# Kernel optimization log

Hardware: AMD Instinct MI355X
Metric: run time of the kernel (lower is better)

Reference implementation:

```python
import jax, jax.numpy as jnp
import numpy as np

HID = 128
N_NODES = 50000
N_EDGES = 640000
N_GRAPHS = 64
N_LAYERS = 3
LN_EPS = 1e-5


def _ln(h, g, b):
    mu = jnp.mean(h, axis=-1, keepdims=True)
    v = jnp.mean(jnp.square(h - mu), axis=-1, keepdims=True)
    return (h - mu) * jax.lax.rsqrt(v + LN_EPS) * g + b


def _mlp2(h, W1, b1, g, be, W2, b2):
    # Linear -> ReLU -> LayerNorm -> (Dropout=identity in eval) -> Linear
    h = _ln(jax.nn.relu(h @ W1.T + b1), g, be)
    return h @ W2.T + b2


def _forward(x, edge_index, batch, axis_W1, axis_b1, axis_g, axis_be, axis_W2, axis_b2, org_W1, org_b1, org_g, org_be, org_W2, org_b2, nin_W, nin_b, conv_W1, conv_b1, conv_g, conv_be, conv_W2, conv_b2, eps, ln_g, ln_b, gate_W1, gate_b1, gate_g, gate_be, gate_W2, gate_b2, head_W1, head_b1, head_g, head_be, head_W2, head_b2):
    axis = x[:, 9:12]
    origin = x[:, 12:15]
    others = jnp.concatenate([x[:, :9], x[:, 15:19]], axis=1)  # [N, 13]
    axis_z = _mlp2(axis, axis_W1, axis_b1, axis_g, axis_be, axis_W2, axis_b2)
    org_z = _mlp2(origin, org_W1, org_b1, org_g, org_be, org_W2, org_b2)
    h = jnp.concatenate([others, axis_z, org_z], axis=1) @ nin_W.T + nin_b  # [N, HID]
    src, dst = edge_index[0], edge_index[1]
    n = x.shape[0]
    for l in range(N_LAYERS):
        res = h
        # GIN: sum-aggregate source features into targets (gather + scatter-add)
        agg = jax.ops.segment_sum(h[src], dst, num_segments=n)
        m = (1.0 + eps[l]) * h + agg
        m = _mlp2(m, conv_W1[l], conv_b1[l], conv_g[l], conv_be[l], conv_W2[l], conv_b2[l])
        h = _ln(jax.nn.relu(m), ln_g[l], ln_b[l]) + res
    # AttentionalAggregation: segment softmax over per-graph node gates
    gate = _mlp2(h, gate_W1, gate_b1, gate_g, gate_be, gate_W2, gate_b2)  # [N, 1]
    gmax = jax.ops.segment_max(gate, batch, num_segments=N_GRAPHS)
    e = jnp.exp(gate - gmax[batch])
    denom = jax.ops.segment_sum(e, batch, num_segments=N_GRAPHS)
    attn = e / denom[batch]
    g = jax.ops.segment_sum(attn * h, batch, num_segments=N_GRAPHS)  # [B, HID]
    logit = _mlp2(g, head_W1, head_b1, head_g, head_be, head_W2, head_b2)[:, 0]
    return logit


def setup_inputs() -> dict:
    key = jax.random.key(0)
    ks = iter(jax.random.split(key, 64))
    nk = lambda: next(ks)
    lin = lambda o, i: jax.random.normal(nk(), (o, i), jnp.float32) / np.float32(np.sqrt(i))
    lin3 = lambda L, o, i: jnp.stack([lin(o, i) for _ in range(L)])
    z = lambda *s: jnp.zeros(s, jnp.float32)
    o = lambda *s: jnp.ones(s, jnp.float32)
    inp = {}
    inp['x'] = jax.random.normal(nk(), (N_NODES, 19), jnp.float32)
    inp['edge_index'] = jax.random.randint(nk(), (2, N_EDGES), 0, N_NODES)
    inp['batch'] = jnp.sort(jax.random.randint(nk(), (N_NODES,), 0, N_GRAPHS))
    for p in ('axis', 'org'):
        inp[p + '_W1'] = lin(16, 3); inp[p + '_b1'] = z(16)
        inp[p + '_g'] = o(16); inp[p + '_be'] = z(16)
        inp[p + '_W2'] = lin(16, 16); inp[p + '_b2'] = z(16)
    inp['nin_W'] = lin(HID, 45); inp['nin_b'] = z(HID)
    inp['conv_W1'] = lin3(N_LAYERS, HID, HID); inp['conv_b1'] = z(N_LAYERS, HID)
    inp['conv_g'] = o(N_LAYERS, HID); inp['conv_be'] = z(N_LAYERS, HID)
    inp['conv_W2'] = lin3(N_LAYERS, HID, HID); inp['conv_b2'] = z(N_LAYERS, HID)
    inp['eps'] = z(N_LAYERS)
    inp['ln_g'] = o(N_LAYERS, HID); inp['ln_b'] = z(N_LAYERS, HID)
    for p in ('gate', 'head'):
        inp[p + '_W1'] = lin(HID // 2, HID); inp[p + '_b1'] = z(HID // 2)
        inp[p + '_g'] = o(HID // 2); inp[p + '_be'] = z(HID // 2)
        inp[p + '_W2'] = lin(1, HID // 2); inp[p + '_b2'] = z(1)
    return inp


def reference(x, edge_index, batch, axis_W1, axis_b1, axis_g, axis_be, axis_W2, axis_b2, org_W1, org_b1, org_g, org_be, org_W2, org_b2, nin_W, nin_b, conv_W1, conv_b1, conv_g, conv_be, conv_W2, conv_b2, eps, ln_g, ln_b, gate_W1, gate_b1, gate_g, gate_be, gate_W2, gate_b2, head_W1, head_b1, head_g, head_be, head_W2, head_b2):
    return _forward(x, edge_index, batch, axis_W1, axis_b1, axis_g, axis_be, axis_W2, axis_b2, org_W1, org_b1, org_g, org_be, org_W2, org_b2, nin_W, nin_b, conv_W1, conv_b1, conv_g, conv_be, conv_W2, conv_b2, eps, ln_g, ln_b, gate_W1, gate_b1, gate_g, gate_be, gate_W2, gate_b2, head_W1, head_b1, head_g, head_be, head_W2, head_b2)
```

## Files before the change

### kernel.cpp

```cpp
#include <hip/hip_runtime.h>

#define N_NODESC 50000
#define N_EDGESC 640000
#define N_GRAPHSC 64
#define HIDC 128
#define LN_EPSF 1e-5f
#define POOL_SPLIT 16
#define SCAN_NB 49
#define EGRID ((N_EDGESC + 255) / 256)
#define NGRID_GB ((N_NODESC + 255) / 256)

typedef short bf16x8 __attribute__((ext_vector_type(8)));
typedef float f32x4 __attribute__((ext_vector_type(4)));

static __device__ __forceinline__ unsigned ord_enc(float f) {
  unsigned u = __float_as_uint(f);
  return (u & 0x80000000u) ? ~u : (u | 0x80000000u);
}
static __device__ __forceinline__ float ord_dec(unsigned u) {
  return __uint_as_float((u & 0x80000000u) ? (u ^ 0x80000000u) : ~u);
}
static __device__ __forceinline__ unsigned short f2bf(float x) {
  unsigned u = __float_as_uint(x);
  u += 0x7fffu + ((u >> 16) & 1u);
  return (unsigned short)(u >> 16);
}
static __device__ __forceinline__ float bf2f(unsigned short b) {
  return __uint_as_float(((unsigned)b) << 16);
}

static __device__ __forceinline__ void mlp16(float in0, float in1, float in2,
    const float* __restrict__ W1, const float* __restrict__ b1,
    const float* __restrict__ g, const float* __restrict__ be,
    const float* __restrict__ W2, const float* __restrict__ b2,
    float* __restrict__ out) {
  float h[16];
  float s1 = 0.f, s2 = 0.f;
#pragma unroll
  for (int j = 0; j < 16; ++j) {
    float v = b1[j] + W1[j*3+0]*in0 + W1[j*3+1]*in1 + W1[j*3+2]*in2;
    v = fmaxf(v, 0.f);
    h[j] = v; s1 += v; s2 += v*v;
  }
  float mu = s1 * (1.f/16.f);
  float var = fmaxf(s2 * (1.f/16.f) - mu*mu, 0.f);
  float rs = rsqrtf(var + LN_EPSF);
  float z[16];
#pragma unroll
  for (int j = 0; j < 16; ++j) z[j] = (h[j]-mu)*rs*g[j] + be[j];
#pragma unroll
  for (int j = 0; j < 16; ++j) {
    float v = b2[j];
#pragma unroll
    for (int k = 0; k < 16; ++k) v += W2[j*16+k]*z[k];
    out[j] = v;
  }
}

__global__ __launch_bounds__(256) void hist_gbound_kernel(const int* __restrict__ ei,
    int* __restrict__ deg, const int* __restrict__ batch, int* __restrict__ gstart) {
  const int b = blockIdx.x;
  if (b < EGRID) {
    int e = b * 256 + threadIdx.x;
    if (e < N_EDGESC) atomicAdd(&deg[ei[N_EDGESC + e]], 1);
  } else {
    int i = (b - EGRID) * 256 + threadIdx.x;
    if (i >= N_NODESC) return;
    int bb = batch[i];
    int prev = (i == 0) ? -1 : batch[i-1];
    for (int g = prev + 1; g <= bb; ++g) gstart[g] = i;
    if (i == N_NODESC - 1) {
      for (int g = bb + 1; g <= N_GRAPHSC; ++g) gstart[g] = N_NODESC;
    }
  }
}

__global__ __launch_bounds__(1024) void scan1_kernel(const int* __restrict__ deg,
                                                     int* __restrict__ incl,
                                                     int* __restrict__ bsum) {
  const int b = blockIdx.x, t = threadIdx.x;
  const int i = b * 1024 + t;
  const int lane = t & 63, w = t >> 6;
  int v = (i < N_NODESC) ? deg[i] : 0;
#pragma unroll
  for (int off = 1; off < 64; off <<= 1) {
    int n = __shfl_up(v, off);
    if (lane >= off) v += n;
  }
  __shared__ int wsum[16];
  if (lane == 63) wsum[w] = v;
  __syncthreads();
  if (t == 0) {
    int run = 0;
#pragma unroll
    for (int k = 0; k < 16; ++k) { int x = wsum[k]; wsum[k] = run; run += x; }
  }
  __syncthreads();
  v += wsum[w];
  if (i < N_NODESC) incl[i] = v;
  if (t == 1023) bsum[b] = v;
}

__global__ __launch_bounds__(1024) void scan23_kernel(const int* __restrict__ deg,
                                                      const int* __restrict__ bsum,
                                                      int* __restrict__ rowptr,
                                                      int* __restrict__ cursor) {
  __shared__ int ex[SCAN_NB + 1];
  const int b = blockIdx.x, t = threadIdx.x;
  if (t < 64) {
    int v = (t < SCAN_NB) ? bsum[t] : 0;
    const int orig = v;
#pragma unroll
    for (int off = 1; off < 64; off <<= 1) {
      int n = __shfl_up(v, off);
      if (t >= off) v += n;
    }
    if (t < SCAN_NB) ex[t] = v - orig;
    if (t == SCAN_NB - 1) ex[SCAN_NB] = v;
  }
  __syncthreads();
  const int i = b * 1024 + t;
  if (i < N_NODESC) {
    int excl = rowptr[i] - deg[i] + ex[b];
    rowptr[i] = excl;
    cursor[i] = excl;
  }
  if (b == 0 && t == 0) rowptr[N_NODESC] = ex[SCAN_NB];
}

__global__ __launch_bounds__(256) void scatter_kernel(const int* __restrict__ ei,
                                                      int* __restrict__ cursor,
                                                      int* __restrict__ esrc) {
  int e = blockIdx.x * 256 + threadIdx.x;
  if (e < N_EDGESC) {
    int d = ei[N_EDGESC + e];
    int slot = atomicAdd(&cursor[d], 1);
    esrc[slot] = ei[e];
  }
}

__global__ __launch_bounds__(128) void enc_kernel(
    const float* __restrict__ x,
    const float* __restrict__ aW1, const float* __restrict__ ab1,
    const float* __restrict__ ag,  const float* __restrict__ abe,
    const float* __restrict__ aW2, const float* __restrict__ ab2,
    const float* __restrict__ oW1, const float* __restrict__ ob1,
    const float* __restrict__ og,  const float* __restrict__ obe,
    const float* __restrict__ oW2, const float* __restrict__ ob2,
    const float* __restrict__ ninW, const float* __restrict__ ninb,
    unsigned short* __restrict__ Hb) {
  __shared__ float sa[48*68];
  __shared__ float sw[48*132];
  const int t = threadIdx.x;
  const int lane = t & 63, w = t >> 6;
  const int nb = blockIdx.x * 64;

  if (t < 64) {
    float in45[45];
    const int gn = nb + t;
    if (gn < N_NODESC) {
      const float* xr = x + gn * 19;
#pragma unroll
      for (int k = 0; k < 9; ++k) in45[k] = xr[k];
#pragma unroll
      for (int k = 0; k < 4; ++k) in45[9+k] = xr[15+k];
      mlp16(xr[9], xr[10], xr[11], aW1, ab1, ag, abe, aW2, ab2, &in45[13]);
      mlp16(xr[12], xr[13], xr[14], oW1, ob1, og, obe, oW2, ob2, &in45[29]);
    } else {
#pragma unroll
      for (int k = 0; k < 45; ++k) in45[k] = 0.f;
    }
#pragma unroll
    for (int k = 0; k < 45; ++k) sa[k*68 + t] = in45[k];
#pragma unroll
    for (int k = 45; k < 48; ++k) sa[k*68 + t] = 0.f;
  }
  for (int idx = t; idx < 48*128; idx += 128) {
    int k = idx >> 7, f = idx & 127;
    sw[k*132 + f] = (k < 45) ? ninW[f*45 + k] : 0.f;
  }
  __syncthreads();

  const int n0 = (lane & 7) * 8;
  const int f0 = ((lane >> 3) << 3) + w * 64;
  float acc[8][8];
#pragma unroll
  for (int i = 0; i < 8; ++i)
#pragma unroll
    for (int j = 0; j < 8; ++j) acc[i][j] = 0.f;

#pragma unroll 4
  for (int k = 0; k < 48; ++k) {
    float av[8], wv[8];
    float4 a0 = *(const float4*)&sa[k*68 + n0];
    float4 a1 = *(const float4*)&sa[k*68 + n0 + 4];
    float4 w0 = *(const float4*)&sw[k*132 + f0];
    float4 w1 = *(const float4*)&sw[k*132 + f0 + 4];
    av[0]=a0.x; av[1]=a0.y; av[2]=a0.z; av[3]=a0.w;
    av[4]=a1.x; av[5]=a1.y; av[6]=a1.z; av[7]=a1.w;
    wv[0]=w0.x; wv[1]=w0.y; wv[2]=w0.z; wv[3]=w0.w;
    wv[4]=w1.x; wv[5]=w1.y; wv[6]=w1.z; wv[7]=w1.w;
#pragma unroll
    for (int i = 0; i < 8; ++i)
#pragma unroll
      for (int j = 0; j < 8; ++j) acc[i][j] += av[i]*wv[j];
  }
  float bb[8];
#pragma unroll
  for (int j = 0; j < 8; ++j) bb[j] = ninb[f0+j];
#pragma unroll
  for (int i = 0; i < 8; ++i) {
    int gn = nb + n0 + i;
    if (gn < N_NODESC) {
      bf16x8 o8;
#pragma unroll
      for (int j = 0; j < 8; ++j) o8[j] = (short)f2bf(acc[i][j] + bb[j]);
      *(bf16x8*)&Hb[gn*HIDC + f0] = o8;
    }
  }
}

__global__ __launch_bounds__(256, 3) void conv_fused_kernel(
    const unsigned short* __restrict__ Hin,
    const int* __restrict__ rowptr, const int* __restrict__ esrc,
    const float* __restrict__ epsp,
    const float* __restrict__ W1, const float* __restrict__ b1,
    const float* __restrict__ g1, const float* __restrict__ be1,
    const float* __restrict__ W2, const float* __restrict__ b2,
    const float* __restrict__ lng, const float* __restrict__ lnb,
    unsigned short* __restrict__ Hout) {
  __shared__ unsigned short Ab[64*136];
  __shared__ unsigned short Wl[128*136];
  const int t = threadIdx.x;
  const int nb = blockIdx.x * 64;

#pragma unroll
  for (int i = 0; i < 16; ++i) {
    int q = t + i*256;
    int f = q >> 5, c4 = q & 31;
    float4 v = *(const float4*)&W1[f*HIDC + c4*4];
    ushort4 h;
    h.x = f2bf(v.x); h.y = f2bf(v.y); h.z = f2bf(v.z); h.w = f2bf(v.w);
    *(ushort4*)&Wl[f*136 + c4*4] = h;
  }

  {
    const float e1 = 1.0f + epsp[0];
    const int v64 = t >> 2;
    const int c   = t & 3;
    const int node = nb + v64;
    if (node < N_NODESC) {
      const unsigned short* __restrict__ hrow = &Hin[node*HIDC + c*32];
      float acc[4][8];
#pragma unroll
      for (int j = 0; j < 4; ++j)
#pragma unroll
        for (int k = 0; k < 8; ++k) acc[j][k] = 0.f;
      int s = rowptr[node];
      const int e = rowptr[node+1];
      for (; s + 2 <= e; s += 2) {
        int i0 = esrc[s], i1 = esrc[s+1];
        const unsigned short* r0 = &Hin[i0*HIDC + c*32];
        const unsigned short* r1 = &Hin[i1*HIDC + c*32];
        bf16x8 x00 = *(const bf16x8*)&r0[0],  x01 = *(const bf16x8*)&r0[8];
        bf16x8 x02 = *(const bf16x8*)&r0[16], x03 = *(const bf16x8*)&r0[24];
        bf16x8 x10 = *(const bf16x8*)&r1[0],  x11 = *(const bf16x8*)&r1[8];
        bf16x8 x12 = *(const bf16x8*)&r1[16], x13 = *(const bf16x8*)&r1[24];
#pragma unroll
        for (int k = 0; k < 8; ++k) {
          acc[0][k] += bf2f((unsigned short)x00[k]) + bf2f((unsigned short)x10[k]);
          acc[1][k] += bf2f((unsigned short)x01[k]) + bf2f((unsigned short)x11[k]);
          acc[2][k] += bf2f((unsigned short)x02[k]) + bf2f((unsigned short)x12[k]);
          acc[3][k] += bf2f((unsigned short)x03[k]) + bf2f((unsigned short)x13[k]);
        }
      }
      if (s < e) {
        const unsigned short* r0 = &Hin[esrc[s]*HIDC + c*32];
        bf16x8 x00 = *(const bf16x8*)&r0[0],  x01 = *(const bf16x8*)&r0[8];
        bf16x8 x02 = *(const bf16x8*)&r0[16], x03 = *(const bf16x8*)&r0[24];
#pragma unroll
        for (int k = 0; k < 8; ++k) {
          acc[0][k] += bf2f((unsigned short)x00[k]);
          acc[1][k] += bf2f((unsigned short)x01[k]);
          acc[2][k] += bf2f((unsigned short)x02[k]);
          acc[3][k] += bf2f((unsigned short)x03[k]);
        }
      }
#pragma unroll
      for (int j = 0; j < 4; ++j) {
        bf16x8 h = *(const bf16x8*)&hrow[j*8];
        bf16x8 m8;
#pragma unroll
        for (int k = 0; k < 8; ++k)
          m8[k] = (short)f2bf(e1*bf2f((unsigned short)h[k]) + acc[j][k]);
        *(bf16x8*)&Ab[v64*136 + c*32 + j*8] = m8;
      }
    } else {
#pragma unroll
      for (int j = 0; j < 4; ++j)
        *(bf16x8*)&Ab[v64*136 + c*32 + j*8] = (bf16x8){0,0,0,0,0,0,0,0};
    }
  }
  __syncthreads();

  const int lane = t & 63, wv = t >> 6;
  const int quad = lane >> 4, l16 = lane & 15;
  const int arow = (wv*16 + l16)*136 + quad*8;

  f32x4 acc[8];
#pragma unroll
  for (int ft = 0; ft < 8; ++ft) acc[ft] = (f32x4){0.f,0.f,0.f,0.f};
#pragma unroll
  for (int ks = 0; ks < 4; ++ks) {
    bf16x8 a = *(const bf16x8*)(const void*)&Ab[arow + ks*32];
#pragma unroll
    for (int ft = 0; ft < 8; ++ft) {
      bf16x8 b = *(const bf16x8*)(const void*)&Wl[(ft*16 + l16)*136 + quad*8 + ks*32];
      acc[ft] = __builtin_amdgcn_mfma_f32_16x16x32_bf16(a, b, acc[ft], 0, 0, 0);
    }
  }

  {
    float bb[8], gg[8], bee[8];
#pragma unroll
    for (int ft = 0; ft < 8; ++ft) {
      int f = ft*16 + l16;
      bb[ft] = b1[f]; gg[ft] = g1[f]; bee[ft] = be1[f];
    }
    float s1[4] = {0,0,0,0}, s2[4] = {0,0,0,0};
#pragma unroll
    for (int ft = 0; ft < 8; ++ft)
#pragma unroll
      for (int r = 0; r < 4; ++r) {
        float v = fmaxf(acc[ft][r] + bb[ft], 0.f);
        acc[ft][r] = v; s1[r] += v; s2[r] += v*v;
      }
#pragma unroll
    for (int m = 1; m < 16; m <<= 1)
#pragma unroll
      for (int r = 0; r < 4; ++r) {
        s1[r] += __shfl_xor(s1[r], m);
        s2[r] += __shfl_xor(s2[r], m);
      }
    float mu[4], rs[4];
#pragma unroll
    for (int r = 0; r < 4; ++r) {
      mu[r] = s1[r] * (1.f/128.f);
      float var = fmaxf(s2[r] * (1.f/128.f) - mu[r]*mu[r], 0.f);
      rs[r] = rsqrtf(var + LN_EPSF);
    }
    __syncthreads();
#pragma unroll
    for (int r = 0; r < 4; ++r) {
      int nloc = wv*16 + quad*4 + r;
#pragma unroll
      for (int ft = 0; ft < 8; ++ft) {
        float o = (acc[ft][r] - mu[r])*rs[r]*gg[ft] + bee[ft];
        Ab[nloc*136 + ft*16 + l16] = f2bf(o);
      }
    }
  }
#pragma unroll
  for (int i = 0; i < 16; ++i) {
    int q = t + i*256;
    int f = q >> 5, c4 = q & 31;
    float4 v = *(const float4*)&W2[f*HIDC + c4*4];
    ushort4 h;
    h.x = f2bf(v.x); h.y = f2bf(v.y); h.z = f2bf(v.z); h.w = f2bf(v.w);
    *(ushort4*)&Wl[f*136 + c4*4] = h;
  }
  __syncthreads();

#pragma unroll
  for (int ft = 0; ft < 8; ++ft) acc[ft] = (f32x4){0.f,0.f,0.f,0.f};
#pragma unroll
  for (int ks = 0; ks < 4; ++ks) {
    bf16x8 a = *(const bf16x8*)(const void*)&Ab[arow + ks*32];
#pragma unroll
    for (int ft = 0; ft < 8; ++ft) {
      bf16x8 b = *(const bf16x8*)(const void*)&Wl[(ft*16 + l16)*136 + quad*8 + ks*32];
      acc[ft] = __builtin_amdgcn_mfma_f32_16x16x32_bf16(a, b, acc[ft], 0, 0, 0);
    }
  }

  {
    float bb[8], gg[8], bee[8];
#pragma unroll
    for (int ft = 0; ft < 8; ++ft) {
      int f = ft*16 + l16;
      bb[ft] = b2[f]; gg[ft] = lng[f]; bee[ft] = lnb[f];
    }
    float s1[4] = {0,0,0,0}, s2[4] = {0,0,0,0};
#pragma unroll
    for (int ft = 0; ft < 8; ++ft)
#pragma unroll
      for (int r = 0; r < 4; ++r) {
        float v = fmaxf(acc[ft][r] + bb[ft], 0.f);
        acc[ft][r] = v; s1[r] += v; s2[r] += v*v;
      }
#pragma unroll
    for (int m = 1; m < 16; m <<= 1)
#pragma unroll
      for (int r = 0; r < 4; ++r) {
        s1[r] += __shfl_xor(s1[r], m);
        s2[r] += __shfl_xor(s2[r], m);
      }
    float mu[4], rs[4];
#pragma unroll
    for (int r = 0; r < 4; ++r) {
      mu[r] = s1[r] * (1.f/128.f);
      float var = fmaxf(s2[r] * (1.f/128.f) - mu[r]*mu[r], 0.f);
      rs[r] = rsqrtf(var + LN_EPSF);
    }
    __syncthreads();
#pragma unroll
    for (int r = 0; r < 4; ++r) {
      int nloc = wv*16 + quad*4 + r;
#pragma unroll
      for (int ft = 0; ft < 8; ++ft) {
        float o = (acc[ft][r] - mu[r])*rs[r]*gg[ft] + bee[ft];
        Ab[nloc*136 + ft*16 + l16] = f2bf(o);
      }
    }
  }
  __syncthreads();
#pragma unroll
  for (int i = 0; i < 4; ++i) {
    int chunk = t + i*256;
    int n = chunk >> 4, cc = chunk & 15;
    int gn = nb + n;
    if (gn >= N_NODESC) continue;
    bf16x8 vv = *(const bf16x8*)&Ab[n*136 + cc*8];
    bf16x8 rr = *(const bf16x8*)&Hin[gn*HIDC + cc*8];
    bf16x8 o8;
#pragma unroll
    for (int k = 0; k < 8; ++k)
      o8[k] = (short)f2bf(bf2f((unsigned short)vv[k]) + bf2f((unsigned short)rr[k]));
    *(bf16x8*)&Hout[gn*HIDC + cc*8] = o8;
  }
}

__global__ __launch_bounds__(256, 4) void gate_mfma_kernel(
    const unsigned short* __restrict__ Hb, const float* __restrict__ W1,
    const float* __restrict__ b1, const float* __restrict__ lng,
    const float* __restrict__ lnb, const float* __restrict__ W2,
    const float* __restrict__ b2, const int* __restrict__ batch,
    float* __restrict__ gateb, unsigned* __restrict__ gmaxu) {
  __shared__ unsigned short Ab[64*136];
  __shared__ unsigned short Wl[64*136];
  __shared__ unsigned sgm[N_GRAPHSC];
  const int t = threadIdx.x;
  const int nb = blockIdx.x * 64;
  if (t < N_GRAPHSC) sgm[t] = 0u;
#pragma unroll
  for (int i = 0; i < 4; ++i) {
    int chunk = t + i*256;
    int n = chunk >> 4, c8 = chunk & 15;
    int gn = nb + n;
    bf16x8 v = {0,0,0,0,0,0,0,0};
    if (gn < N_NODESC) v = *(const bf16x8*)&Hb[gn*HIDC + c8*8];
    *(bf16x8*)&Ab[n*136 + c8*8] = v;
  }
#pragma unroll
  for (int i = 0; i < 8; ++i) {
    int q = t + i*256;
    int f = q >> 5, c4 = q & 31;
    float4 v = *(const float4*)&W1[f*HIDC + c4*4];
    ushort4 h;
    h.x = f2bf(v.x); h.y = f2bf(v.y); h.z = f2bf(v.z); h.w = f2bf(v.w);
    *(ushort4*)&Wl[f*136 + c4*4] = h;
  }
  __syncthreads();

  const int lane = t & 63, wv = t >> 6;
  const int quad = lane >> 4, l16 = lane & 15;
  f32x4 acc[4];
#pragma unroll
  for (int ft = 0; ft < 4; ++ft) acc[ft] = (f32x4){0.f,0.f,0.f,0.f};

  const int arow = (wv*16 + l16)*136 + quad*8;
#pragma unroll
  for (int ks = 0; ks < 4; ++ks) {
    bf16x8 a = *(const bf16x8*)(const void*)&Ab[arow + ks*32];
#pragma unroll
    for (int ft = 0; ft < 4; ++ft) {
      bf16x8 b = *(const bf16x8*)(const void*)&Wl[(ft*16 + l16)*136 + quad*8 + ks*32];
      acc[ft] = __builtin_amdgcn_mfma_f32_16x16x32_bf16(a, b, acc[ft], 0, 0, 0);
    }
  }

  float bb[4], gg[4], bee[4], w2v[4];
#pragma unroll
  for (int ft = 0; ft < 4; ++ft) {
    int f = ft*16 + l16;
    bb[ft] = b1[f]; gg[ft] = lng[f]; bee[ft] = lnb[f]; w2v[ft] = W2[f];
  }
  float s1[4] = {0,0,0,0}, s2[4] = {0,0,0,0};
#pragma unroll
  for (int ft = 0; ft < 4; ++ft)
#pragma unroll
    for (int r = 0; r < 4; ++r) {
      float v = fmaxf(acc[ft][r] + bb[ft], 0.f);
      acc[ft][r] = v; s1[r] += v; s2[r] += v*v;
    }
#pragma unroll
  for (int m = 1; m < 16; m <<= 1)
#pragma unroll
    for (int r = 0; r < 4; ++r) {
      s1[r] += __shfl_xor(s1[r], m);
      s2[r] += __shfl_xor(s2[r], m);
    }
  float pd[4];
#pragma unroll
  for (int r = 0; r < 4; ++r) {
    float mu = s1[r] * (1.f/64.f);
    float var = fmaxf(s2[r] * (1.f/64.f) - mu*mu, 0.f);
    float rs = rsqrtf(var + LN_EPSF);
    float p = 0.f;
#pragma unroll
    for (int ft = 0; ft < 4; ++ft)
      p += ((acc[ft][r] - mu)*rs*gg[ft] + bee[ft]) * w2v[ft];
    pd[r] = p;
  }
#pragma unroll
  for (int m = 1; m < 16; m <<= 1)
#pragma unroll
    for (int r = 0; r < 4; ++r) pd[r] += __shfl_xor(pd[r], m);
  if (l16 == 0) {
    float b2v = b2[0];
#pragma unroll
    for (int r = 0; r < 4; ++r) {
      int node = nb + wv*16 + quad*4 + r;
      if (node < N_NODESC) {
        float gv = pd[r] + b2v;
        gateb[node] = gv;
        atomicMax(&sgm[batch[node]], ord_enc(gv));
      }
    }
  }
  __syncthreads();
  if (t < N_GRAPHSC && sgm[t] != 0u) atomicMax(&gmaxu[t], sgm[t]);
}

__global__ __launch_bounds__(256) void pool_kernel(const unsigned short* __restrict__ Hb,
    const float* __restrict__ gateb, const int* __restrict__ gstart,
    const unsigned* __restrict__ gmaxu, float* __restrict__ S,
    float* __restrict__ denom) {
  const int g    = blockIdx.x / POOL_SPLIT;
  const int part = blockIdx.x % POOL_SPLIT;
  const int s0 = gstart[g], s1 = gstart[g+1];
  const int cnt = s1 - s0;
  const int chunk = (cnt + POOL_SPLIT - 1) / POOL_SPLIT;
  int lo = s0 + part * chunk;
  int hi = lo + chunk; if (hi > s1) hi = s1;
  const int t = threadIdx.x;
  const int c8 = t & 15;
  const int v  = t >> 4;
  const float gm = ord_dec(gmaxu[g]);
  float acc[8];
#pragma unroll
  for (int k = 0; k < 8; ++k) acc[k] = 0.f;
  float de = 0.f;
  for (int n = lo + v; n < hi; n += 16) {
    float e = expf(gateb[n] - gm);
    bf16x8 hv = *(const bf16x8*)&Hb[n*HIDC + c8*8];
#pragma unroll
    for (int k = 0; k < 8; ++k) acc[k] += e * bf2f((unsigned short)hv[k]);
    if (c8 == 0) de += e;
  }
  __shared__ float sacc[16*128];
  __shared__ float sden[16];
#pragma unroll
  for (int k = 0; k < 8; ++k) sacc[v*128 + c8*8 + k] = acc[k];
  if (c8 == 0) sden[v] = de;
  __syncthreads();
  if (t < 128) {
    float s = 0.f;
#pragma unroll
    for (int vv = 0; vv < 16; ++vv) s += sacc[vv*128 + t];
    atomicAdd(&S[g*HIDC + t], s);
  }
  if (t == 0) {
    float d = 0.f;
#pragma unroll
    for (int vv = 0; vv < 16; ++vv) d += sden[vv];
    atomicAdd(&denom[g], d);
  }
}

__global__ __launch_bounds__(64) void head_kernel(const float* __restrict__ S,
    const float* __restrict__ denom, const float* __restrict__ W1,
    const float* __restrict__ b1, const float* __restrict__ g,
    const float* __restrict__ be, const float* __restrict__ W2,
    const float* __restrict__ b2, float* __restrict__ out) {
  const int gr = blockIdx.x;
  const int j = threadIdx.x;
  const float inv = 1.0f / denom[gr];
  float v = b1[j];
  for (int k = 0; k < HIDC; ++k) v += (S[gr*HIDC + k] * inv) * W1[j*HIDC + k];
  v = fmaxf(v, 0.f);
  float s1 = v, s2 = v*v;
  for (int off = 32; off; off >>= 1) { s1 += __shfl_xor(s1, off); s2 += __shfl_xor(s2, off); }
  float mu = s1 * (1.f/64.f);
  float var = fmaxf(s2 * (1.f/64.f) - mu*mu, 0.f);
  float rs = rsqrtf(var + LN_EPSF);
  float z = (v-mu)*rs*g[j] + be[j];
  float p = z * W2[j];
  for (int off = 32; off; off >>= 1) p += __shfl_xor(p, off);
  if (j == 0) out[gr] = p + b2[0];
}

extern "C" void kernel_launch(void* const* d_in, const int* in_sizes, int n_in,
                              void* d_out, int out_size, void* d_ws, size_t ws_size,
                              hipStream_t stream) {
  (void)in_sizes; (void)n_in; (void)out_size; (void)ws_size;
  const float* x     = (const float*)d_in[0];
  const int*   ei    = (const int*)d_in[1];
  const int*   batch = (const int*)d_in[2];
  const float* aW1 = (const float*)d_in[3];
  const float* ab1 = (const float*)d_in[4];
  const float* ag  = (const float*)d_in[5];
  const float* abe = (const float*)d_in[6];
  const float* aW2 = (const float*)d_in[7];
  const float* ab2 = (const float*)d_in[8];
  const float* oW1 = (const float*)d_in[9];
  const float* ob1 = (const float*)d_in[10];
  const float* og  = (const float*)d_in[11];
  const float* obe = (const float*)d_in[12];
  const float* oW2 = (const float*)d_in[13];
  const float* ob2 = (const float*)d_in[14];
  const float* ninW = (const float*)d_in[15];
  const float* ninb = (const float*)d_in[16];
  const float* cW1 = (const float*)d_in[17];
  const float* cb1 = (const float*)d_in[18];
  const float* cg  = (const float*)d_in[19];
  const float* cbe = (const float*)d_in[20];
  const float* cW2 = (const float*)d_in[21];
  const float* cb2 = (const float*)d_in[22];
  const float* eps = (const float*)d_in[23];
  const float* lng = (const float*)d_in[24];
  const float* lnb = (const float*)d_in[25];
  const float* gW1 = (const float*)d_in[26];
  const float* gb1 = (const float*)d_in[27];
  const float* gg  = (const float*)d_in[28];
  const float* gbe = (const float*)d_in[29];
  const float* gW2 = (const float*)d_in[30];
  const float* gb2 = (const float*)d_in[31];
  const float* hW1 = (const float*)d_in[32];
  const float* hb1 = (const float*)d_in[33];
  const float* hg  = (const float*)d_in[34];
  const float* hbe = (const float*)d_in[35];
  const float* hW2 = (const float*)d_in[36];
  const float* hb2 = (const float*)d_in[37];

  char* ws = (char*)d_ws;
  unsigned short* Ha = (unsigned short*)(ws + 0);
  unsigned short* Hc = (unsigned short*)(ws + 12800000);
  float* gateb = (float*)(ws + 25600000);
  int*   deg   = (int*)(ws + 25800000);
  float* S     = (float*)(ws + 26000000);
  float* denom = (float*)(ws + 26032768);
  unsigned* gmaxu = (unsigned*)(ws + 26033024);
  int* rowptr  = (int*)(ws + 26033280);
  int* cursor  = (int*)(ws + 26233284);
  int* esrc    = (int*)(ws + 26433284);
  int* bsum    = (int*)(ws + 28993284);
  int* gstart  = (int*)(ws + 28993540);

  hipMemsetAsync(deg, 0, 233280, stream);

  hist_gbound_kernel<<<EGRID + NGRID_GB, 256, 0, stream>>>(ei, deg, batch, gstart);
  scan1_kernel<<<SCAN_NB, 1024, 0, stream>>>(deg, rowptr, bsum);
  scan23_kernel<<<SCAN_NB, 1024, 0, stream>>>(deg, bsum, rowptr, cursor);
  scatter_kernel<<<EGRID, 256, 0, stream>>>(ei, cursor, esrc);

  const int ngrid64 = (N_NODESC + 63) / 64;
  enc_kernel<<<ngrid64, 128, 0, stream>>>(x, aW1, ab1, ag, abe, aW2, ab2,
                                          oW1, ob1, og, obe, oW2, ob2,
                                          ninW, ninb, Ha);
  unsigned short* cur = Ha;
  unsigned short* nxt = Hc;
  for (int l = 0; l < 3; ++l) {
    conv_fused_kernel<<<ngrid64, 256, 0, stream>>>(
        cur, rowptr, esrc, eps + l,
        cW1 + l*HIDC*HIDC, cb1 + l*HIDC, cg + l*HIDC, cbe + l*HIDC,
        cW2 + l*HIDC*HIDC, cb2 + l*HIDC, lng + l*HIDC, lnb + l*HIDC,
        nxt);
    unsigned short* tmp = cur; cur = nxt; nxt = tmp;
  }
  gate_mfma_kernel<<<ngrid64, 256, 0, stream>>>(cur, gW1, gb1, gg, gbe, gW2, gb2,
                                                batch, gateb, gmaxu);
  pool_kernel<<<N_GRAPHSC * POOL_SPLIT, 256, 0, stream>>>(cur, gateb, gstart, gmaxu, S, denom);
  head_kernel<<<N_GRAPHSC, 64, 0, stream>>>(S, denom, hW1, hb1, hg, hbe, hW2, hb2,
                                            (float*)d_out);
}
```

Baseline: 396.8 us.

## Pre-convert weights to bf16 once and read MFMA B operands from global

Adds a small prep kernel that converts the conv and gate weight matrices to bf16 once per call. The conv and gate kernels then read MFMA B fragments directly from global/L2 instead of each block converting fp32 weights into a large LDS tile. This removes the per-block weight staging and conversion and shrinks LDS use, and the launch bounds rise to 6 waves-per-EU to gain occupancy. The cost is uncoalesced per-lane global loads of weights in the inner MFMA loop, which now depend on cache hits, and possible register pressure under the tighter bound.

```diff
diff --git a/kernel.cpp b/kernel.cpp
--- a/kernel.cpp
+++ b/kernel.cpp
@@ -55,6 +55,17 @@
     for (int k = 0; k < 16; ++k) v += W2[j*16+k]*z[k];
     out[j] = v;
   }
+}
+
+__global__ __launch_bounds__(256) void wprep_kernel(
+    const float* __restrict__ cW1, const float* __restrict__ cW2,
+    const float* __restrict__ gW1,
+    unsigned short* __restrict__ Wb1, unsigned short* __restrict__ Wb2,
+    unsigned short* __restrict__ gWb) {
+  int i = blockIdx.x * 256 + threadIdx.x;
+  if (i < 49152) Wb1[i] = f2bf(cW1[i]);
+  else if (i < 98304) Wb2[i - 49152] = f2bf(cW2[i - 49152]);
+  else if (i < 106496) gWb[i - 98304] = f2bf(gW1[i - 98304]);
 }
 
 __global__ __launch_bounds__(256) void hist_gbound_kernel(const int* __restrict__ ei,
@@ -220,29 +231,18 @@
   }
 }
 
-__global__ __launch_bounds__(256, 3) void conv_fused_kernel(
+__global__ __launch_bounds__(256, 6) void conv_fused_kernel(
     const unsigned short* __restrict__ Hin,
     const int* __restrict__ rowptr, const int* __restrict__ esrc,
     const float* __restrict__ epsp,
-    const float* __restrict__ W1, const float* __restrict__ b1,
+    const unsigned short* __restrict__ W1b, const float* __restrict__ b1,
     const float* __restrict__ g1, const float* __restrict__ be1,
-    const float* __restrict__ W2, const float* __restrict__ b2,
+    const unsigned short* __restrict__ W2b, const float* __restrict__ b2,
     const float* __restrict__ lng, const float* __restrict__ lnb,
     unsigned short* __restrict__ Hout) {
   __shared__ unsigned short Ab[64*136];
-  __shared__ unsigned short Wl[128*136];
   const int t = threadIdx.x;
   const int nb = blockIdx.x * 64;
-
-#pragma unroll
-  for (int i = 0; i < 16; ++i) {
-    int q = t + i*256;
-    int f = q >> 5, c4 = q & 31;
-    float4 v = *(const float4*)&W1[f*HIDC + c4*4];
-    ushort4 h;
-    h.x = f2bf(v.x); h.y = f2bf(v.y); h.z = f2bf(v.z); h.w = f2bf(v.w);
-    *(ushort4*)&Wl[f*136 + c4*4] = h;
-  }
 
   {
     const float e1 = 1.0f + epsp[0];
@@ -306,6 +306,7 @@
   const int lane = t & 63, wv = t >> 6;
   const int quad = lane >> 4, l16 = lane & 15;
   const int arow = (wv*16 + l16)*136 + quad*8;
+  const int brow_base = l16*HIDC + quad*8;
 
   f32x4 acc[8];
 #pragma unroll
@@ -315,7 +316,7 @@
     bf16x8 a = *(const bf16x8*)(const void*)&Ab[arow + ks*32];
 #pragma unroll
     for (int ft = 0; ft < 8; ++ft) {
-      bf16x8 b = *(const bf16x8*)(const void*)&Wl[(ft*16 + l16)*136 + quad*8 + ks*32];
+      bf16x8 b = *(const bf16x8*)&W1b[brow_base + ft*16*HIDC + ks*32];
       acc[ft] = __builtin_amdgcn_mfma_f32_16x16x32_bf16(a, b, acc[ft], 0, 0, 0);
     }
   }
@@ -360,15 +361,6 @@
       }
     }
   }
-#pragma unroll
-  for (int i = 0; i < 16; ++i) {
-    int q = t + i*256;
-    int f = q >> 5, c4 = q & 31;
-    float4 v = *(const float4*)&W2[f*HIDC + c4*4];
-    ushort4 h;
-    h.x = f2bf(v.x); h.y = f2bf(v.y); h.z = f2bf(v.z); h.w = f2bf(v.w);
-    *(ushort4*)&Wl[f*136 + c4*4] = h;
-  }
   __syncthreads();
 
 #pragma unroll
@@ -378,7 +370,7 @@
     bf16x8 a = *(const bf16x8*)(const void*)&Ab[arow + ks*32];
 #pragma unroll
     for (int ft = 0; ft < 8; ++ft) {
-      bf16x8 b = *(const bf16x8*)(const void*)&Wl[(ft*16 + l16)*136 + quad*8 + ks*32];
+      bf16x8 b = *(const bf16x8*)&W2b[brow_base + ft*16*HIDC + ks*32];
       acc[ft] = __builtin_amdgcn_mfma_f32_16x16x32_bf16(a, b, acc[ft], 0, 0, 0);
     }
   }
@@ -440,14 +432,13 @@
   }
 }
 
-__global__ __launch_bounds__(256, 4) void gate_mfma_kernel(
-    const unsigned short* __restrict__ Hb, const float* __restrict__ W1,
+__global__ __launch_bounds__(256, 6) void gate_mfma_kernel(
+    const unsigned short* __restrict__ Hb, const unsigned short* __restrict__ W1b,
     const float* __restrict__ b1, const float* __restrict__ lng,
     const float* __restrict__ lnb, const float* __restrict__ W2,
     const float* __restrict__ b2, const int* __restrict__ batch,
     float* __restrict__ gateb, unsigned* __restrict__ gmaxu) {
   __shared__ unsigned short Ab[64*136];
-  __shared__ unsigned short Wl[64*136];
   __shared__ unsigned sgm[N_GRAPHSC];
   const int t = threadIdx.x;
   const int nb = blockIdx.x * 64;
@@ -461,15 +452,6 @@
     if (gn < N_NODESC) v = *(const bf16x8*)&Hb[gn*HIDC + c8*8];
     *(bf16x8*)&Ab[n*136 + c8*8] = v;
   }
-#pragma unroll
-  for (int i = 0; i < 8; ++i) {
-    int q = t + i*256;
-    int f = q >> 5, c4 = q & 31;
-    float4 v = *(const float4*)&W1[f*HIDC + c4*4];
-    ushort4 h;
-    h.x = f2bf(v.x); h.y = f2bf(v.y); h.z = f2bf(v.z); h.w = f2bf(v.w);
-    *(ushort4*)&Wl[f*136 + c4*4] = h;
-  }
   __syncthreads();
 
   const int lane = t & 63, wv = t >> 6;
@@ -479,12 +461,13 @@
   for (int ft = 0; ft < 4; ++ft) acc[ft] = (f32x4){0.f,0.f,0.f,0.f};
 
   const int arow = (wv*16 + l16)*136 + quad*8;
+  const int brow_base = l16*HIDC + quad*8;
 #pragma unroll
   for (int ks = 0; ks < 4; ++ks) {
     bf16x8 a = *(const bf16x8*)(const void*)&Ab[arow + ks*32];
 #pragma unroll
     for (int ft = 0; ft < 4; ++ft) {
-      bf16x8 b = *(const bf16x8*)(const void*)&Wl[(ft*16 + l16)*136 + quad*8 + ks*32];
+      bf16x8 b = *(const bf16x8*)&W1b[brow_base + ft*16*HIDC + ks*32];
       acc[ft] = __builtin_amdgcn_mfma_f32_16x16x32_bf16(a, b, acc[ft], 0, 0, 0);
     }
   }
@@ -666,9 +649,13 @@
   int* esrc    = (int*)(ws + 26433284);
   int* bsum    = (int*)(ws + 28993284);
   int* gstart  = (int*)(ws + 28993540);
+  unsigned short* Wb1 = (unsigned short*)(ws + 29000000);
+  unsigned short* Wb2 = (unsigned short*)(ws + 29100000);
+  unsigned short* gWb = (unsigned short*)(ws + 29200000);
 
   hipMemsetAsync(deg, 0, 233280, stream);
 
+  wprep_kernel<<<(106496 + 255) / 256, 256, 0, stream>>>(cW1, cW2, gW1, Wb1, Wb2, gWb);
   hist_gbound_kernel<<<EGRID + NGRID_GB, 256, 0, stream>>>(ei, deg, batch, gstart);
   scan1_kernel<<<SCAN_NB, 1024, 0, stream>>>(deg, rowptr, bsum);
   scan23_kernel<<<SCAN_NB, 1024, 0, stream>>>(deg, bsum, rowptr, cursor);
@@ -683,12 +670,12 @@
   for (int l = 0; l < 3; ++l) {
     conv_fused_kernel<<<ngrid64, 256, 0, stream>>>(
         cur, rowptr, esrc, eps + l,
-        cW1 + l*HIDC*HIDC, cb1 + l*HIDC, cg + l*HIDC, cbe + l*HIDC,
-        cW2 + l*HIDC*HIDC, cb2 + l*HIDC, lng + l*HIDC, lnb + l*HIDC,
+        Wb1 + l*HIDC*HIDC, cb1 + l*HIDC, cg + l*HIDC, cbe + l*HIDC,
+        Wb2 + l*HIDC*HIDC, cb2 + l*HIDC, lng + l*HIDC, lnb + l*HIDC,
         nxt);
     unsigned short* tmp = cur; cur = nxt; nxt = tmp;
   }
-  gate_mfma_kernel<<<ngrid64, 256, 0, stream>>>(cur, gW1, gb1, gg, gbe, gW2, gb2,
+  gate_mfma_kernel<<<ngrid64, 256, 0, stream>>>(cur, gWb, gb1, gg, gbe, gW2, gb2,
                                                 batch, gateb, gmaxu);
   pool_kernel<<<N_GRAPHSC * POOL_SPLIT, 256, 0, stream>>>(cur, gateb, gstart, gmaxu, S, denom);
   head_kernel<<<N_GRAPHSC, 64, 0, stream>>>(S, denom, hW1, hb1, hg, hbe, hW2, hb2,
```

Result: slower. 440.4 us (+11.0%).

## Fuse CSR build into cooperative kernel and use MFMA for node encoder

Applied to the files above, without the earlier changes.

Replaces the memset, histogram, two scan kernels and scatter with a single cooperative kernel that uses grid-wide syncs. The same kernel also zeroes the pooling buffers and pre-converts the input projection weight to bf16. The node encoder GEMM is moved from FP32 FMA to bf16 MFMA, with an LDS-staged coalesced store. The aim is to cut launch overhead and encoder compute, at the cost of grid-sync latency, limited parallelism for the edge passes, and bf16 rounding of the encoder inputs.

```diff
diff --git a/kernel.cpp b/kernel.cpp
--- a/kernel.cpp
+++ b/kernel.cpp
@@ -1,4 +1,7 @@
 #include <hip/hip_runtime.h>
+#include <hip/hip_cooperative_groups.h>
+
+namespace cg = cooperative_groups;
 
 #define N_NODESC 50000
 #define N_EDGESC 640000
@@ -6,9 +9,6 @@
 #define HIDC 128
 #define LN_EPSF 1e-5f
 #define POOL_SPLIT 16
-#define SCAN_NB 49
-#define EGRID ((N_EDGESC + 255) / 256)
-#define NGRID_GB ((N_NODESC + 255) / 256)
 
 typedef short bf16x8 __attribute__((ext_vector_type(8)));
 typedef float f32x4 __attribute__((ext_vector_type(4)));
@@ -57,89 +57,95 @@
   }
 }
 
-__global__ __launch_bounds__(256) void hist_gbound_kernel(const int* __restrict__ ei,
-    int* __restrict__ deg, const int* __restrict__ batch, int* __restrict__ gstart) {
-  const int b = blockIdx.x;
-  if (b < EGRID) {
-    int e = b * 256 + threadIdx.x;
-    if (e < N_EDGESC) atomicAdd(&deg[ei[N_EDGESC + e]], 1);
-  } else {
-    int i = (b - EGRID) * 256 + threadIdx.x;
-    if (i >= N_NODESC) return;
+__global__ __launch_bounds__(256) void csr_coop_kernel(
+    const int* __restrict__ ei, const int* __restrict__ batch,
+    const float* __restrict__ ninW,
+    int* __restrict__ deg, int* __restrict__ rowptr, int* __restrict__ cursor,
+    int* __restrict__ esrc, int* __restrict__ bsum, int* __restrict__ gstart,
+    float* __restrict__ S, float* __restrict__ denom,
+    unsigned* __restrict__ gmaxu, unsigned short* __restrict__ ninWb) {
+  cg::grid_group grid = cg::this_grid();
+  const int b = blockIdx.x, t = threadIdx.x;
+  const int gid = b * 256 + t;
+  const int GSZ = 256 * 256;
+  __shared__ int wsum[4];
+  __shared__ int sb[256];
+
+  for (int i = gid; i < N_NODESC; i += GSZ) deg[i] = 0;
+  for (int i = gid; i < N_GRAPHSC*HIDC; i += GSZ) S[i] = 0.f;
+  if (gid < N_GRAPHSC) { denom[gid] = 0.f; gmaxu[gid] = 0u; }
+  for (int i = gid; i < 128*64; i += GSZ) {
+    int f = i >> 6, k = i & 63;
+    ninWb[i] = (k < 45) ? f2bf(ninW[f*45 + k]) : (unsigned short)0;
+  }
+  for (int i = gid; i < N_NODESC; i += GSZ) {
     int bb = batch[i];
     int prev = (i == 0) ? -1 : batch[i-1];
     for (int g = prev + 1; g <= bb; ++g) gstart[g] = i;
-    if (i == N_NODESC - 1) {
+    if (i == N_NODESC - 1)
       for (int g = bb + 1; g <= N_GRAPHSC; ++g) gstart[g] = N_NODESC;
-    }
-  }
-}
-
-__global__ __launch_bounds__(1024) void scan1_kernel(const int* __restrict__ deg,
-                                                     int* __restrict__ incl,
-                                                     int* __restrict__ bsum) {
-  const int b = blockIdx.x, t = threadIdx.x;
-  const int i = b * 1024 + t;
-  const int lane = t & 63, w = t >> 6;
-  int v = (i < N_NODESC) ? deg[i] : 0;
-#pragma unroll
-  for (int off = 1; off < 64; off <<= 1) {
-    int n = __shfl_up(v, off);
-    if (lane >= off) v += n;
-  }
-  __shared__ int wsum[16];
-  if (lane == 63) wsum[w] = v;
-  __syncthreads();
-  if (t == 0) {
-    int run = 0;
-#pragma unroll
-    for (int k = 0; k < 16; ++k) { int x = wsum[k]; wsum[k] = run; run += x; }
-  }
-  __syncthreads();
-  v += wsum[w];
-  if (i < N_NODESC) incl[i] = v;
-  if (t == 1023) bsum[b] = v;
-}
-
-__global__ __launch_bounds__(1024) void scan23_kernel(const int* __restrict__ deg,
-                                                      const int* __restrict__ bsum,
-                                                      int* __restrict__ rowptr,
-                                                      int* __restrict__ cursor) {
-  __shared__ int ex[SCAN_NB + 1];
-  const int b = blockIdx.x, t = threadIdx.x;
-  if (t < 64) {
-    int v = (t < SCAN_NB) ? bsum[t] : 0;
-    const int orig = v;
+  }
+  grid.sync();
+
+  for (int e = gid; e < N_EDGESC; e += GSZ) atomicAdd(&deg[ei[N_EDGESC + e]], 1);
+  grid.sync();
+
+  {
+    const int i = gid;
+    int v = (i < N_NODESC) ? deg[i] : 0;
+    const int lane = t & 63, w = t >> 6;
 #pragma unroll
     for (int off = 1; off < 64; off <<= 1) {
       int n = __shfl_up(v, off);
-      if (t >= off) v += n;
-    }
-    if (t < SCAN_NB) ex[t] = v - orig;
-    if (t == SCAN_NB - 1) ex[SCAN_NB] = v;
-  }
-  __syncthreads();
-  const int i = b * 1024 + t;
-  if (i < N_NODESC) {
-    int excl = rowptr[i] - deg[i] + ex[b];
-    rowptr[i] = excl;
-    cursor[i] = excl;
-  }
-  if (b == 0 && t == 0) rowptr[N_NODESC] = ex[SCAN_NB];
-}
-
-__global__ __launch_bounds__(256) void scatter_kernel(const int* __restrict__ ei,
-                                                      int* __restrict__ cursor,
-                                                      int* __restrict__ esrc) {
-  int e = blockIdx.x * 256 + threadIdx.x;
-  if (e < N_EDGESC) {
+      if (lane >= off) v += n;
+    }
+    if (lane == 63) wsum[w] = v;
+    __syncthreads();
+    if (t == 0) {
+      int run = 0;
+#pragma unroll
+      for (int k = 0; k < 4; ++k) { int x = wsum[k]; wsum[k] = run; run += x; }
+    }
+    __syncthreads();
+    v += wsum[w];
+    if (i < N_NODESC) rowptr[i] = v;
+    if (t == 255) bsum[b] = v;
+  }
+  grid.sync();
+
+  if (b == 0) {
+    int v = bsum[t];
+    sb[t] = v;
+    __syncthreads();
+    for (int off = 1; off < 256; off <<= 1) {
+      int n = (t >= off) ? sb[t - off] : 0;
+      __syncthreads();
+      sb[t] += n;
+      __syncthreads();
+    }
+    bsum[t] = sb[t] - v;
+    if (t == 255) rowptr[N_NODESC] = sb[255];
+  }
+  grid.sync();
+
+  {
+    const int i = gid;
+    if (i < N_NODESC) {
+      int excl = rowptr[i] - deg[i] + bsum[b];
+      rowptr[i] = excl;
+      cursor[i] = excl;
+    }
+  }
+  grid.sync();
+
+  for (int e = gid; e < N_EDGESC; e += GSZ) {
     int d = ei[N_EDGESC + e];
     int slot = atomicAdd(&cursor[d], 1);
     esrc[slot] = ei[e];
   }
 }
 
-__global__ __launch_bounds__(128) void enc_kernel(
+__global__ __launch_bounds__(256, 4) void enc_mfma_kernel(
     const float* __restrict__ x,
     const float* __restrict__ aW1, const float* __restrict__ ab1,
     const float* __restrict__ ag,  const float* __restrict__ abe,
@@ -147,18 +153,17 @@
     const float* __restrict__ oW1, const float* __restrict__ ob1,
     const float* __restrict__ og,  const float* __restrict__ obe,
     const float* __restrict__ oW2, const float* __restrict__ ob2,
-    const float* __restrict__ ninW, const float* __restrict__ ninb,
+    const unsigned short* __restrict__ ninWb, const float* __restrict__ ninb,
     unsigned short* __restrict__ Hb) {
-  __shared__ float sa[48*68];
-  __shared__ float sw[48*132];
+  __shared__ unsigned short Ab[64*136];
   const int t = threadIdx.x;
-  const int lane = t & 63, w = t >> 6;
   const int nb = blockIdx.x * 64;
 
   if (t < 64) {
-    float in45[45];
     const int gn = nb + t;
+    unsigned short row[64];
     if (gn < N_NODESC) {
+      float in45[45];
       const float* xr = x + gn * 19;
 #pragma unroll
       for (int k = 0; k < 9; ++k) in45[k] = xr[k];
@@ -166,57 +171,53 @@
       for (int k = 0; k < 4; ++k) in45[9+k] = xr[15+k];
       mlp16(xr[9], xr[10], xr[11], aW1, ab1, ag, abe, aW2, ab2, &in45[13]);
       mlp16(xr[12], xr[13], xr[14], oW1, ob1, og, obe, oW2, ob2, &in45[29]);
+#pragma unroll
+      for (int k = 0; k < 45; ++k) row[k] = f2bf(in45[k]);
+#pragma unroll
+      for (int k = 45; k < 64; ++k) row[k] = 0;
     } else {
 #pragma unroll
-      for (int k = 0; k < 45; ++k) in45[k] = 0.f;
-    }
-#pragma unroll
-    for (int k = 0; k < 45; ++k) sa[k*68 + t] = in45[k];
-#pragma unroll
-    for (int k = 45; k < 48; ++k) sa[k*68 + t] = 0.f;
-  }
-  for (int idx = t; idx < 48*128; idx += 128) {
-    int k = idx >> 7, f = idx & 127;
-    sw[k*132 + f] = (k < 45) ? ninW[f*45 + k] : 0.f;
-  }
-  __syncthreads();
-
-  const int n0 = (lane & 7) * 8;
-  const int f0 = ((lane >> 3) << 3) + w * 64;
-  float acc[8][8];
-#pragma unroll
-  for (int i = 0; i < 8; ++i)
-#pragma unroll
-    for (int j = 0; j < 8; ++j) acc[i][j] = 0.f;
-
-#pragma unroll 4
-  for (int k = 0; k < 48; ++k) {
-    float av[8], wv[8];
-    float4 a0 = *(const float4*)&sa[k*68 + n0];
-    float4 a1 = *(const float4*)&sa[k*68 + n0 + 4];
-    float4 w0 = *(const float4*)&sw[k*132 + f0];
-    float4 w1 = *(const float4*)&sw[k*132 + f0 + 4];
-    av[0]=a0.x; av[1]=a0.y; av[2]=a0.z; av[3]=a0.w;
-    av[4]=a1.x; av[5]=a1.y; av[6]=a1.z; av[7]=a1.w;
-    wv[0]=w0.x; wv[1]=w0.y; wv[2]=w0.z; wv[3]=w0.w;
-    wv[4]=w1.x; wv[5]=w1.y; wv[6]=w1.z; wv[7]=w1.w;
-#pragma unroll
-    for (int i = 0; i < 8; ++i)
-#pragma unroll
-      for (int j = 0; j < 8; ++j) acc[i][j] += av[i]*wv[j];
+      for (int k = 0; k < 64; ++k) row[k] = 0;
+    }
+#pragma unroll
+    for (int k = 0; k < 64; ++k) Ab[t*136 + k] = row[k];
+  }
+  __syncthreads();
+
+  const int lane = t & 63, wv = t >> 6;
+  const int quad = lane >> 4, l16 = lane & 15;
+  const int arow = (wv*16 + l16)*136 + quad*8;
+  f32x4 acc[8];
+#pragma unroll
+  for (int ft = 0; ft < 8; ++ft) acc[ft] = (f32x4){0.f,0.f,0.f,0.f};
+#pragma unroll
+  for (int ks = 0; ks < 2; ++ks) {
+    bf16x8 a = *(const bf16x8*)(const void*)&Ab[arow + ks*32];
+#pragma unroll
+    for (int ft = 0; ft < 8; ++ft) {
+      bf16x8 bfr = *(const bf16x8*)&ninWb[(ft*16 + l16)*64 + quad*8 + ks*32];
+      acc[ft] = __builtin_amdgcn_mfma_f32_16x16x32_bf16(a, bfr, acc[ft], 0, 0, 0);
+    }
   }
   float bb[8];
 #pragma unroll
-  for (int j = 0; j < 8; ++j) bb[j] = ninb[f0+j];
-#pragma unroll
-  for (int i = 0; i < 8; ++i) {
-    int gn = nb + n0 + i;
-    if (gn < N_NODESC) {
-      bf16x8 o8;
-#pragma unroll
-      for (int j = 0; j < 8; ++j) o8[j] = (short)f2bf(acc[i][j] + bb[j]);
-      *(bf16x8*)&Hb[gn*HIDC + f0] = o8;
-    }
+  for (int ft = 0; ft < 8; ++ft) bb[ft] = ninb[ft*16 + l16];
+  __syncthreads();
+#pragma unroll
+  for (int r = 0; r < 4; ++r) {
+    int nloc = wv*16 + quad*4 + r;
+#pragma unroll
+    for (int ft = 0; ft < 8; ++ft)
+      Ab[nloc*136 + ft*16 + l16] = f2bf(acc[ft][r] + bb[ft]);
+  }
+  __syncthreads();
+#pragma unroll
+  for (int i = 0; i < 4; ++i) {
+    int chunk = t + i*256;
+    int n = chunk >> 4, c8 = chunk & 15;
+    int gn = nb + n;
+    if (gn < N_NODESC)
+      *(bf16x8*)&Hb[gn*HIDC + c8*8] = *(const bf16x8*)&Ab[n*136 + c8*8];
   }
 }
 
@@ -665,19 +666,24 @@
   int* cursor  = (int*)(ws + 26233284);
   int* esrc    = (int*)(ws + 26433284);
   int* bsum    = (int*)(ws + 28993284);
-  int* gstart  = (int*)(ws + 28993540);
-
-  hipMemsetAsync(deg, 0, 233280, stream);
-
-  hist_gbound_kernel<<<EGRID + NGRID_GB, 256, 0, stream>>>(ei, deg, batch, gstart);
-  scan1_kernel<<<SCAN_NB, 1024, 0, stream>>>(deg, rowptr, bsum);
-  scan23_kernel<<<SCAN_NB, 1024, 0, stream>>>(deg, bsum, rowptr, cursor);
-  scatter_kernel<<<EGRID, 256, 0, stream>>>(ei, cursor, esrc);
+  int* gstart  = (int*)(ws + 28994308);
+  unsigned short* ninWb = (unsigned short*)(ws + 29000000);
+
+  {
+    void* cargs[] = {
+      (void*)&ei, (void*)&batch, (void*)&ninW,
+      (void*)&deg, (void*)&rowptr, (void*)&cursor, (void*)&esrc,
+      (void*)&bsum, (void*)&gstart,
+      (void*)&S, (void*)&denom, (void*)&gmaxu, (void*)&ninWb
+    };
+    hipLaunchCooperativeKernel((void*)csr_coop_kernel, dim3(256), dim3(256),
+                               cargs, 0, stream);
+  }
 
   const int ngrid64 = (N_NODESC + 63) / 64;
-  enc_kernel<<<ngrid64, 128, 0, stream>>>(x, aW1, ab1, ag, abe, aW2, ab2,
-                                          oW1, ob1, og, obe, oW2, ob2,
-                                          ninW, ninb, Ha);
+  enc_mfma_kernel<<<ngrid64, 256, 0, stream>>>(x, aW1, ab1, ag, abe, aW2, ab2,
+                                               oW1, ob1, og, obe, oW2, ob2,
+                                               ninWb, ninb, Ha);
   unsigned short* cur = Ha;
   unsigned short* nxt = Hc;
   for (int l = 0; l < 3; ++l) {
```

After: 569.8 us. +43.6%, slower.

## Use bf16 MFMA for node-input encoder projection with prepacked weights

Applied to the files above, without the earlier changes.

Replaces the scalar FP32 shared-memory GEMM in the encoder (45->128 projection) with bf16 MFMA 16x16x32 instructions. The nin weight matrix is converted to padded bf16 once, in extra blocks of the histogram kernel, so encoder blocks no longer transpose the fp32 weights into LDS. Outputs are staged through LDS for coalesced row stores. The inputs to the projection are now rounded to bf16, which adds some precision loss, and the first 64 threads still run the small MLPs serially.

```diff
diff --git a/kernel.cpp b/kernel.cpp
--- a/kernel.cpp
+++ b/kernel.cpp
@@ -9,6 +9,7 @@
 #define SCAN_NB 49
 #define EGRID ((N_EDGESC + 255) / 256)
 #define NGRID_GB ((N_NODESC + 255) / 256)
+#define WPREP_NB 32
 
 typedef short bf16x8 __attribute__((ext_vector_type(8)));
 typedef float f32x4 __attribute__((ext_vector_type(4)));
@@ -58,12 +59,13 @@
 }
 
 __global__ __launch_bounds__(256) void hist_gbound_kernel(const int* __restrict__ ei,
-    int* __restrict__ deg, const int* __restrict__ batch, int* __restrict__ gstart) {
+    int* __restrict__ deg, const int* __restrict__ batch, int* __restrict__ gstart,
+    const float* __restrict__ ninW, unsigned short* __restrict__ ninWb) {
   const int b = blockIdx.x;
   if (b < EGRID) {
     int e = b * 256 + threadIdx.x;
     if (e < N_EDGESC) atomicAdd(&deg[ei[N_EDGESC + e]], 1);
-  } else {
+  } else if (b < EGRID + NGRID_GB) {
     int i = (b - EGRID) * 256 + threadIdx.x;
     if (i >= N_NODESC) return;
     int bb = batch[i];
@@ -71,6 +73,12 @@
     for (int g = prev + 1; g <= bb; ++g) gstart[g] = i;
     if (i == N_NODESC - 1) {
       for (int g = bb + 1; g <= N_GRAPHSC; ++g) gstart[g] = N_NODESC;
+    }
+  } else {
+    int i = (b - EGRID - NGRID_GB) * 256 + threadIdx.x;
+    if (i < 128*64) {
+      int f = i >> 6, k = i & 63;
+      ninWb[i] = (k < 45) ? f2bf(ninW[f*45 + k]) : (unsigned short)0;
     }
   }
 }
@@ -139,7 +147,7 @@
   }
 }
 
-__global__ __launch_bounds__(128) void enc_kernel(
+__global__ __launch_bounds__(256, 4) void enc_mfma_kernel(
     const float* __restrict__ x,
     const float* __restrict__ aW1, const float* __restrict__ ab1,
     const float* __restrict__ ag,  const float* __restrict__ abe,
@@ -147,18 +155,17 @@
     const float* __restrict__ oW1, const float* __restrict__ ob1,
     const float* __restrict__ og,  const float* __restrict__ obe,
     const float* __restrict__ oW2, const float* __restrict__ ob2,
-    const float* __restrict__ ninW, const float* __restrict__ ninb,
+    const unsigned short* __restrict__ ninWb, const float* __restrict__ ninb,
     unsigned short* __restrict__ Hb) {
-  __shared__ float sa[48*68];
-  __shared__ float sw[48*132];
+  __shared__ unsigned short Ab[64*136];
   const int t = threadIdx.x;
-  const int lane = t & 63, w = t >> 6;
   const int nb = blockIdx.x * 64;
 
   if (t < 64) {
-    float in45[45];
     const int gn = nb + t;
+    unsigned short row[64];
     if (gn < N_NODESC) {
+      float in45[45];
       const float* xr = x + gn * 19;
 #pragma unroll
       for (int k = 0; k < 9; ++k) in45[k] = xr[k];
@@ -166,57 +173,53 @@
       for (int k = 0; k < 4; ++k) in45[9+k] = xr[15+k];
       mlp16(xr[9], xr[10], xr[11], aW1, ab1, ag, abe, aW2, ab2, &in45[13]);
       mlp16(xr[12], xr[13], xr[14], oW1, ob1, og, obe, oW2, ob2, &in45[29]);
+#pragma unroll
+      for (int k = 0; k < 45; ++k) row[k] = f2bf(in45[k]);
+#pragma unroll
+      for (int k = 45; k < 64; ++k) row[k] = 0;
     } else {
 #pragma unroll
-      for (int k = 0; k < 45; ++k) in45[k] = 0.f;
-    }
-#pragma unroll
-    for (int k = 0; k < 45; ++k) sa[k*68 + t] = in45[k];
-#pragma unroll
-    for (int k = 45; k < 48; ++k) sa[k*68 + t] = 0.f;
-  }
-  for (int idx = t; idx < 48*128; idx += 128) {
-    int k = idx >> 7, f = idx & 127;
-    sw[k*132 + f] = (k < 45) ? ninW[f*45 + k] : 0.f;
-  }
-  __syncthreads();
-
-  const int n0 = (lane & 7) * 8;
-  const int f0 = ((lane >> 3) << 3) + w * 64;
-  float acc[8][8];
-#pragma unroll
-  for (int i = 0; i < 8; ++i)
-#pragma unroll
-    for (int j = 0; j < 8; ++j) acc[i][j] = 0.f;
-
-#pragma unroll 4
-  for (int k = 0; k < 48; ++k) {
-    float av[8], wv[8];
-    float4 a0 = *(const float4*)&sa[k*68 + n0];
-    float4 a1 = *(const float4*)&sa[k*68 + n0 + 4];
-    float4 w0 = *(const float4*)&sw[k*132 + f0];
-    float4 w1 = *(const float4*)&sw[k*132 + f0 + 4];
-    av[0]=a0.x; av[1]=a0.y; av[2]=a0.z; av[3]=a0.w;
-    av[4]=a1.x; av[5]=a1.y; av[6]=a1.z; av[7]=a1.w;
-    wv[0]=w0.x; wv[1]=w0.y; wv[2]=w0.z; wv[3]=w0.w;
-    wv[4]=w1.x; wv[5]=w1.y; wv[6]=w1.z; wv[7]=w1.w;
-#pragma unroll
-    for (int i = 0; i < 8; ++i)
-#pragma unroll
-      for (int j = 0; j < 8; ++j) acc[i][j] += av[i]*wv[j];
+      for (int k = 0; k < 64; ++k) row[k] = 0;
+    }
+#pragma unroll
+    for (int k = 0; k < 64; ++k) Ab[t*136 + k] = row[k];
+  }
+  __syncthreads();
+
+  const int lane = t & 63, wv = t >> 6;
+  const int quad = lane >> 4, l16 = lane & 15;
+  const int arow = (wv*16 + l16)*136 + quad*8;
+  f32x4 acc[8];
+#pragma unroll
+  for (int ft = 0; ft < 8; ++ft) acc[ft] = (f32x4){0.f,0.f,0.f,0.f};
+#pragma unroll
+  for (int ks = 0; ks < 2; ++ks) {
+    bf16x8 a = *(const bf16x8*)(const void*)&Ab[arow + ks*32];
+#pragma unroll
+    for (int ft = 0; ft < 8; ++ft) {
+      bf16x8 bfr = *(const bf16x8*)&ninWb[(ft*16 + l16)*64 + quad*8 + ks*32];
+      acc[ft] = __builtin_amdgcn_mfma_f32_16x16x32_bf16(a, bfr, acc[ft], 0, 0, 0);
+    }
   }
   float bb[8];
 #pragma unroll
-  for (int j = 0; j < 8; ++j) bb[j] = ninb[f0+j];
-#pragma unroll
-  for (int i = 0; i < 8; ++i) {
-    int gn = nb + n0 + i;
-    if (gn < N_NODESC) {
-      bf16x8 o8;
-#pragma unroll
-      for (int j = 0; j < 8; ++j) o8[j] = (short)f2bf(acc[i][j] + bb[j]);
-      *(bf16x8*)&Hb[gn*HIDC + f0] = o8;
-    }
+  for (int ft = 0; ft < 8; ++ft) bb[ft] = ninb[ft*16 + l16];
+  __syncthreads();
+#pragma unroll
+  for (int r = 0; r < 4; ++r) {
+    int nloc = wv*16 + quad*4 + r;
+#pragma unroll
+    for (int ft = 0; ft < 8; ++ft)
+      Ab[nloc*136 + ft*16 + l16] = f2bf(acc[ft][r] + bb[ft]);
+  }
+  __syncthreads();
+#pragma unroll
+  for (int i = 0; i < 4; ++i) {
+    int chunk = t + i*256;
+    int n = chunk >> 4, c8 = chunk & 15;
+    int gn = nb + n;
+    if (gn < N_NODESC)
+      *(bf16x8*)&Hb[gn*HIDC + c8*8] = *(const bf16x8*)&Ab[n*136 + c8*8];
   }
 }
 
@@ -666,18 +669,20 @@
   int* esrc    = (int*)(ws + 26433284);
   int* bsum    = (int*)(ws + 28993284);
   int* gstart  = (int*)(ws + 28993540);
+  unsigned short* ninWb = (unsigned short*)(ws + 29000000);
 
   hipMemsetAsync(deg, 0, 233280, stream);
 
-  hist_gbound_kernel<<<EGRID + NGRID_GB, 256, 0, stream>>>(ei, deg, batch, gstart);
+  hist_gbound_kernel<<<EGRID + NGRID_GB + WPREP_NB, 256, 0, stream>>>(
+      ei, deg, batch, gstart, ninW, ninWb);
   scan1_kernel<<<SCAN_NB, 1024, 0, stream>>>(deg, rowptr, bsum);
   scan23_kernel<<<SCAN_NB, 1024, 0, stream>>>(deg, bsum, rowptr, cursor);
   scatter_kernel<<<EGRID, 256, 0, stream>>>(ei, cursor, esrc);
 
   const int ngrid64 = (N_NODESC + 63) / 64;
-  enc_kernel<<<ngrid64, 128, 0, stream>>>(x, aW1, ab1, ag, abe, aW2, ab2,
-                                          oW1, ob1, og, obe, oW2, ob2,
-                                          ninW, ninb, Ha);
+  enc_mfma_kernel<<<ngrid64, 256, 0, stream>>>(x, aW1, ab1, ag, abe, aW2, ab2,
+                                               oW1, ob1, og, obe, oW2, ob2,
+                                               ninWb, ninb, Ha);
   unsigned short* cur = Ha;
   unsigned short* nxt = Hc;
   for (int l = 0; l < 3; ++l) {
```

New measurement: 387.9 us. 1.02x faster.
